# Performance work log

Measured on AMD Instinct MI355X. Metric: run time of the kernel, lower is better.

The kernel has to match this reference:

```python
import jax, jax.numpy as jnp
import numpy as np

N_NODES = 100000
N_EDGES = 1600000
N_GRAPHS = 512
IN_CH = 64
HID = 128
LAT = 64
MAX_NODES = 128
OUT_SIZE = MAX_NODES * (MAX_NODES - 1) // 2  # 8128


def _gcn_conv(x, W, b, src, dst, n):
    """PyG GCNConv: x' = D^-1/2 (A+I) D^-1/2 (x W) + b, degrees include self-loops."""
    h = x @ W  # [N, out]
    deg = jnp.zeros((n,), h.dtype).at[dst].add(1.0) + 1.0  # in-degree + self-loop
    dinv = jax.lax.rsqrt(deg)
    norm = dinv[src] * dinv[dst]  # [E]
    agg = jnp.zeros_like(h).at[dst].add(h[src] * norm[:, None])  # neighbor scatter-add
    agg = agg + h * (dinv * dinv)[:, None]  # self-loop term, norm = 1/deg
    return agg + b


def setup_inputs() -> dict:
    key = jax.random.key(0)
    ks = jax.random.split(key, 20)
    s = 0.02
    inp = {
        "x": jax.random.normal(ks[0], (N_NODES, IN_CH), jnp.float32),
        "edge_index": jax.random.randint(ks[1], (2, N_EDGES), 0, N_NODES),
        "batch": jnp.sort(jax.random.randint(ks[2], (N_NODES,), 0, N_GRAPHS)),
        "eps": jax.random.normal(ks[3], (N_GRAPHS, LAT), jnp.float32),
        # encoder params
        "W1": jax.random.normal(ks[4], (IN_CH, HID), jnp.float32) * s,
        "b1": jnp.zeros((HID,), jnp.float32),
        "W2": jax.random.normal(ks[5], (HID, HID), jnp.float32) * s,
        "b2": jnp.zeros((HID,), jnp.float32),
        "Wmu": jax.random.normal(ks[6], (HID, LAT), jnp.float32) * s,
        "bmu": jnp.zeros((LAT,), jnp.float32),
        "Wlv": jax.random.normal(ks[7], (HID, LAT), jnp.float32) * s,
        "blv": jnp.zeros((LAT,), jnp.float32),
        # decoder MLP params
        "D1": jax.random.normal(ks[8], (LAT, HID), jnp.float32) * s,
        "d1": jnp.zeros((HID,), jnp.float32),
        "D2": jax.random.normal(ks[9], (HID, HID), jnp.float32) * s,
        "d2": jnp.zeros((HID,), jnp.float32),
        "D3": jax.random.normal(ks[10], (HID, OUT_SIZE), jnp.float32) * s,
        "d3": jnp.zeros((OUT_SIZE,), jnp.float32),
    }
    return inp


def reference(x, edge_index, batch, eps, W1, b1, W2, b2, Wmu, bmu, Wlv, blv,
              D1, d1, D2, d2, D3, d3):
    src, dst = edge_index[0], edge_index[1]
    # --- encoder: two GCN layers + ReLU ---
    h = jax.nn.relu(_gcn_conv(x, W1, b1, src, dst, N_NODES))
    h = jax.nn.relu(_gcn_conv(h, W2, b2, src, dst, N_NODES))
    # --- global mean pool by graph id ---
    sums = jax.ops.segment_sum(h, batch, num_segments=N_GRAPHS)
    cnts = jax.ops.segment_sum(jnp.ones((N_NODES,), h.dtype), batch, num_segments=N_GRAPHS)
    h_graph = sums / jnp.maximum(cnts, 1.0)[:, None]  # [G, HID]
    mu = h_graph @ Wmu + bmu
    logvar = h_graph @ Wlv + blv
    # --- reparameterise ---
    z = mu + eps * jnp.exp(0.5 * logvar)  # [G, LAT]
    # --- MLP decoder -> symmetric adjacency ---
    p = jax.nn.relu(z @ D1 + d1)
    p = jax.nn.relu(p @ D2 + d2)
    probs = jax.nn.sigmoid(p @ D3 + d3)  # [G, OUT_SIZE]
    r, c = jnp.triu_indices(MAX_NODES, k=1)
    adj = jnp.zeros((N_GRAPHS, MAX_NODES, MAX_NODES), probs.dtype)
    adj = adj.at[:, r, c].set(probs)
    adj = adj + jnp.swapaxes(adj, 1, 2)
    return adj, mu, logvar
```

## Files before the change

### kernel.cpp

```cpp
#include <hip/hip_runtime.h>
#include <hip/hip_fp16.h>

#define NN 100000
#define NE 1600000
#define NG 512
#define OUTS 8128
#define NB2 196
#define CHUNK 8192
#define NPB 196

typedef short bf16x8 __attribute__((ext_vector_type(8)));
typedef _Float16 f16x8 __attribute__((ext_vector_type(8)));
typedef _Float16 f16x2 __attribute__((ext_vector_type(2)));
typedef float f32x4 __attribute__((ext_vector_type(4)));

__device__ __forceinline__ unsigned pack_bf16x2(float a, float b) {
    unsigned ua = __float_as_uint(a);
    unsigned ub = __float_as_uint(b);
    ua = (ua + 0x7fffu + ((ua >> 16) & 1u)) >> 16;
    ub = (ub + 0x7fffu + ((ub >> 16) & 1u)) >> 16;
    return ua | (ub << 16);
}
__device__ __forceinline__ unsigned short f2bf(float f) {
    unsigned u = __float_as_uint(f);
    u = (u + 0x7fffu + ((u >> 16) & 1u)) >> 16;
    return (unsigned short)u;
}
__device__ __forceinline__ unsigned cvt_pkrtz_u(float a, float b) {
    auto h = __builtin_amdgcn_cvt_pkrtz(a, b);
    union { decltype(h) h2; unsigned u; } c; c.h2 = h; return c.u;
}
__device__ __forceinline__ f16x2 u2h(unsigned u) { union { unsigned u; f16x2 h; } c; c.u = u; return c.h; }

__device__ __forceinline__ unsigned f2fp8(float f) {
    unsigned h = (unsigned)__half_as_ushort(__float2half(f * 0.00390625f));
    return (h + 0x3Fu + ((h >> 7) & 1u)) >> 7;
}

__global__ __launch_bounds__(512) void k_part(const int* __restrict__ src, const int* __restrict__ dst,
        int* __restrict__ tmp, int* __restrict__ scanhist) {
    __shared__ int hist[NB2], cur[NB2], scan[256];
    int p = blockIdx.x, t = threadIdx.x;
    int e0 = p * CHUNK;
    int e1 = min(e0 + CHUNK, NE);
    for (int i = t; i < NB2; i += 512) hist[i] = 0;
    __syncthreads();
    for (int e = e0 + t; e < e1; e += 512)
        atomicAdd(&hist[dst[e] >> 9], 1);
    __syncthreads();
    int h = 0;
    if (t < 256) { h = (t < NB2) ? hist[t] : 0; scan[t] = h; }
    __syncthreads();
    for (int off = 1; off < 256; off <<= 1) {
        int v = (t < 256 && t >= off) ? scan[t - off] : 0;
        __syncthreads();
        if (t < 256) scan[t] += v;
        __syncthreads();
    }
    if (t < NB2) {
        int excl = scan[t] - h;
        cur[t] = excl;
        scanhist[p * (NB2 + 1) + t] = excl;
    }
    if (t == 0) scanhist[p * (NB2 + 1) + NB2] = e1 - e0;
    __syncthreads();
    for (int e = e0 + t; e < e1; e += 512) {
        int d = dst[e];
        int b = d >> 9;
        int r = atomicAdd(&cur[b], 1);
        tmp[e0 + r] = (src[e] << 9) | (d & 511);
    }
}

__global__ __launch_bounds__(256) void k_btotseg(const int* __restrict__ scanhist,
        int* __restrict__ bucketbase, const int* __restrict__ batch, int* __restrict__ seg_end) {
    if (blockIdx.x == 0) {
        __shared__ int sc[256];
        int b = threadIdx.x;
        int tot = 0;
        if (b < NB2) {
            for (int p = 0; p < NPB; ++p)
                tot += scanhist[p * (NB2 + 1) + b + 1] - scanhist[p * (NB2 + 1) + b];
        }
        sc[b] = tot;
        __syncthreads();
        for (int off = 1; off < 256; off <<= 1) {
            int v = (b >= off) ? sc[b - off] : 0;
            __syncthreads();
            sc[b] += v;
            __syncthreads();
        }
        if (b < NB2) bucketbase[b] = sc[b] - tot;
    } else {
        int i = (blockIdx.x - 1) * 256 + threadIdx.x;
        if (i >= NN) return;
        int b = batch[i];
        int bn = (i == NN - 1) ? NG : batch[i + 1];
        for (int g = b; g < bn; ++g) seg_end[g] = i + 1;
        if (i == 0) {
            for (int g = 0; g < b; ++g) seg_end[g] = 0;
        }
    }
}

__global__ __launch_bounds__(1024) void k_fill2(const int* __restrict__ bucketbase,
        const int* __restrict__ scanhist, const int* __restrict__ tmp,
        int* __restrict__ colidx, int* __restrict__ cnti, int* __restrict__ rowptr,
        float* __restrict__ dinv) {
    __shared__ int lc[512], rb[512], sc[256];
    int b = blockIdx.x, t = threadIdx.x;
    int n0 = b << 9;
    if (t < 512) lc[t] = 0;
    __syncthreads();
    int w = t >> 6, lane = t & 63;
    for (int p = w; p < NPB; p += 16) {
        int s0 = scanhist[p * (NB2 + 1) + b];
        int s1 = scanhist[p * (NB2 + 1) + b + 1];
        int base = p * CHUNK;
        for (int i = s0 + lane; i < s1; i += 64)
            atomicAdd(&lc[tmp[base + i] & 511], 1);
    }
    __syncthreads();
    int v0 = 0, v1 = 0, s = 0;
    if (t < 256) { v0 = lc[2 * t]; v1 = lc[2 * t + 1]; s = v0 + v1; sc[t] = s; }
    __syncthreads();
    for (int off = 1; off < 256; off <<= 1) {
        int x = (t < 256 && t >= off) ? sc[t - off] : 0;
        __syncthreads();
        if (t < 256) sc[t] += x;
        __syncthreads();
    }
    if (t < 256) {
        int excl = sc[t] - s;
        int base0 = bucketbase[b];
        rb[2 * t] = base0 + excl;
        rb[2 * t + 1] = base0 + excl + v0;
        int node0 = n0 + 2 * t;
        if (node0 < NN) {
            cnti[node0] = v0;
            rowptr[node0] = base0 + excl;
            dinv[node0] = rsqrtf((float)v0 + 1.0f);
        }
        if (node0 + 1 < NN) {
            cnti[node0 + 1] = v1;
            rowptr[node0 + 1] = base0 + excl + v0;
            dinv[node0 + 1] = rsqrtf((float)v1 + 1.0f);
        }
    }
    __syncthreads();
    if (t < 512) lc[t] = 0;
    __syncthreads();
    for (int p = w; p < NPB; p += 16) {
        int s0 = scanhist[p * (NB2 + 1) + b];
        int s1 = scanhist[p * (NB2 + 1) + b + 1];
        int base = p * CHUNK;
        for (int i = s0 + lane; i < s1; i += 64) {
            int v = tmp[base + i];
            int dl = v & 511;
            int pos = atomicAdd(&lc[dl], 1);
            colidx[rb[dl] + pos] = v >> 9;
        }
    }
}

__global__ __launch_bounds__(256) void k_wtall(const float* __restrict__ W1,
        const float* __restrict__ W2,
        unsigned short* __restrict__ wt1, unsigned short* __restrict__ wt2) {
    int i = blockIdx.x * 256 + threadIdx.x;
    if (i < 8192) {
        int n = i >> 6, k = i & 63;
        wt1[i] = (unsigned short)__half_as_ushort(__float2half(W1[k * 128 + n]));
    } else if (i < 24576) {
        int e = i - 8192;
        int n = e >> 7, k = e & 127;
        wt2[e] = f2bf(W2[k * 128 + n]);
    }
}

__global__ __launch_bounds__(256) void k_wt3t(const float* __restrict__ D3,
        unsigned short* __restrict__ o) {
    __shared__ float tile[32][33];
    int n0 = blockIdx.x * 32, k0 = blockIdx.y * 32;
    for (int i = threadIdx.x; i < 1024; i += 256) {
        int kk = i >> 5, nn = i & 31;
        tile[kk][nn] = D3[(long)(k0 + kk) * OUTS + n0 + nn];
    }
    __syncthreads();
    for (int i = threadIdx.x; i < 1024; i += 256) {
        int nn = i >> 5, kk = i & 31;
        o[(long)(n0 + nn) * 128 + k0 + kk] =
            (unsigned short)__half_as_ushort(__float2half(tile[kk][nn]));
    }
}

__global__ __launch_bounds__(256) void k_scale_x(const float* __restrict__ x,
        const float* __restrict__ dinv, unsigned* __restrict__ u1) {
    int i = blockIdx.x * 256 + threadIdx.x;
    int row = i >> 5, c = i & 31;
    float2 v = *(const float2*)&x[(long)row * 64 + c * 2];
    float d = dinv[row];
    u1[i] = cvt_pkrtz_u(v.x * d, v.y * d);
}

__global__ __launch_bounds__(256) void k_gather1(const int* __restrict__ rowptr,
        const int* __restrict__ cnti, const int* __restrict__ colidx,
        const unsigned* __restrict__ u, const float* __restrict__ dinv,
        unsigned* __restrict__ s1) {
    int node = blockIdx.x * 32 + (threadIdx.x >> 3);
    int lane = threadIdx.x & 7;
    const uint4* uf = (const uint4*)u;
    uint4 self = uf[node * 8 + lane];
    f16x2 a0 = u2h(self.x), a1 = u2h(self.y), a2 = u2h(self.z), a3 = u2h(self.w);
    f16x2 z = {(_Float16)0.f, (_Float16)0.f};
    f16x2 b0 = z, b1 = z, b2 = z, b3 = z;
    int n = cnti[node];
    const int* ci = colidx + rowptr[node];
    int j = 0;
    for (; j + 4 <= n; j += 4) {
        uint4 va = uf[ci[j] * 8 + lane];
        uint4 vb = uf[ci[j + 1] * 8 + lane];
        uint4 vc = uf[ci[j + 2] * 8 + lane];
        uint4 vd = uf[ci[j + 3] * 8 + lane];
        a0 += u2h(va.x); a1 += u2h(va.y); a2 += u2h(va.z); a3 += u2h(va.w);
        b0 += u2h(vb.x); b1 += u2h(vb.y); b2 += u2h(vb.z); b3 += u2h(vb.w);
        a0 += u2h(vc.x); a1 += u2h(vc.y); a2 += u2h(vc.z); a3 += u2h(vc.w);
        b0 += u2h(vd.x); b1 += u2h(vd.y); b2 += u2h(vd.z); b3 += u2h(vd.w);
    }
    for (; j < n; ++j) {
        uint4 va = uf[ci[j] * 8 + lane];
        a0 += u2h(va.x); a1 += u2h(va.y); a2 += u2h(va.z); a3 += u2h(va.w);
    }
    a0 += b0; a1 += b1; a2 += b2; a3 += b3;
    float d = dinv[node];
    uint4 o;
    o.x = cvt_pkrtz_u((float)a0[0] * d, (float)a0[1] * d);
    o.y = cvt_pkrtz_u((float)a1[0] * d, (float)a1[1] * d);
    o.z = cvt_pkrtz_u((float)a2[0] * d, (float)a2[1] * d);
    o.w = cvt_pkrtz_u((float)a3[0] * d, (float)a3[1] * d);
    *(uint4*)&s1[node * 32 + lane * 4] = o;
}

#define DECO(W, LO, HI) { LO += u2h(((W) & 0x007f007fu) << 7); HI += u2h(((W) & 0x7f007f00u) >> 1); }
__global__ __launch_bounds__(256) void k_gather2(const int* __restrict__ rowptr,
        const int* __restrict__ cnti, const int* __restrict__ colidx,
        const unsigned* __restrict__ u, const float* __restrict__ dinv,
        unsigned* __restrict__ s2) {
    int node = blockIdx.x * 32 + (threadIdx.x >> 3);
    int lane = threadIdx.x & 7;
    const uint4* uf = (const uint4*)u;
    uint4 self = uf[node * 8 + lane];
    f16x2 z = {(_Float16)0.f, (_Float16)0.f};
    f16x2 la0 = z, ha0 = z, la1 = z, ha1 = z, la2 = z, ha2 = z, la3 = z, ha3 = z;
    f16x2 lb0 = z, hb0 = z, lb1 = z, hb1 = z, lb2 = z, hb2 = z, lb3 = z, hb3 = z;
    DECO(self.x, la0, ha0) DECO(self.y, la1, ha1) DECO(self.z, la2, ha2) DECO(self.w, la3, ha3)
    int n = cnti[node];
    const int* ci = colidx + rowptr[node];
    int j = 0;
    for (; j + 4 <= n; j += 4) {
        uint4 va = uf[ci[j] * 8 + lane];
        uint4 vb = uf[ci[j + 1] * 8 + lane];
        uint4 vc = uf[ci[j + 2] * 8 + lane];
        uint4 vd = uf[ci[j + 3] * 8 + lane];
        DECO(va.x, la0, ha0) DECO(va.y, la1, ha1) DECO(va.z, la2, ha2) DECO(va.w, la3, ha3)
        DECO(vb.x, lb0, hb0) DECO(vb.y, lb1, hb1) DECO(vb.z, lb2, hb2) DECO(vb.w, lb3, hb3)
        DECO(vc.x, la0, ha0) DECO(vc.y, la1, ha1) DECO(vc.z, la2, ha2) DECO(vc.w, la3, ha3)
        DECO(vd.x, lb0, hb0) DECO(vd.y, lb1, hb1) DECO(vd.z, lb2, hb2) DECO(vd.w, lb3, hb3)
    }
    for (; j < n; ++j) {
        uint4 va = uf[ci[j] * 8 + lane];
        DECO(va.x, la0, ha0) DECO(va.y, la1, ha1) DECO(va.z, la2, ha2) DECO(va.w, la3, ha3)
    }
    la0 += lb0; ha0 += hb0; la1 += lb1; ha1 += hb1;
    la2 += lb2; ha2 += hb2; la3 += lb3; ha3 += hb3;
    float d = dinv[node] * 16.0f;
    uint4 o1, o2;
    o1.x = pack_bf16x2((float)la0[0] * d, (float)ha0[0] * d);
    o1.y = pack_bf16x2((float)la0[1] * d, (float)ha0[1] * d);
    o1.z = pack_bf16x2((float)la1[0] * d, (float)ha1[0] * d);
    o1.w = pack_bf16x2((float)la1[1] * d, (float)ha1[1] * d);
    o2.x = pack_bf16x2((float)la2[0] * d, (float)ha2[0] * d);
    o2.y = pack_bf16x2((float)la2[1] * d, (float)ha2[1] * d);
    o2.z = pack_bf16x2((float)la3[0] * d, (float)ha3[0] * d);
    o2.w = pack_bf16x2((float)la3[1] * d, (float)ha3[1] * d);
    *(uint4*)&s2[node * 64 + lane * 8] = o1;
    *(uint4*)&s2[node * 64 + lane * 8 + 4] = o2;
}

template<int K, int EPI, int AF16>
__global__ __launch_bounds__(256) void k_gemm_mfma(const unsigned short* __restrict__ Ab,
        const unsigned short* __restrict__ wt, const float* __restrict__ dinv,
        const float* __restrict__ bias, void* __restrict__ outp) {
    constexpr int KS = K / 32;
    constexpr int SLOTS = K / 8;
    __shared__ __align__(16) unsigned short wlds[128 * K];
    char* lb = (char*)wlds;
    for (int c = threadIdx.x; c < 128 * SLOTS; c += 256) {
        int n = c / SLOTS, s = c - n * SLOTS;
        *(uint4*)(lb + n * (2 * K) + ((s ^ (n & 7)) << 4)) = *(const uint4*)(wt + c * 8);
    }
    __syncthreads();
    int lane = threadIdx.x & 63;
    int w = threadIdx.x >> 6;
    int r0 = blockIdx.x * 64 + w * 16;
    int arow = r0 + (lane & 15);
    if (arow >= NN) arow = NN - 1;
    bf16x8 af[KS];
    #pragma unroll
    for (int ks = 0; ks < KS; ++ks)
        af[ks] = *(const bf16x8*)&Ab[(long)arow * K + ks * 32 + (lane >> 4) * 8];
    f32x4 acc[8];
    #pragma unroll
    for (int t = 0; t < 8; ++t) acc[t] = (f32x4){0.f, 0.f, 0.f, 0.f};
    #pragma unroll
    for (int ks = 0; ks < KS; ++ks) {
        #pragma unroll
        for (int t = 0; t < 8; ++t) {
            int n = t * 16 + (lane & 15);
            int slot = ks * 4 + (lane >> 4);
            bf16x8 braw = *(const bf16x8*)(lb + n * (2 * K) + ((slot ^ (n & 7)) << 4));
            if constexpr (AF16) {
                union { bf16x8 r; f16x8 h; } ca, cb;
                ca.r = af[ks]; cb.r = braw;
                acc[t] = __builtin_amdgcn_mfma_f32_16x16x32_f16(ca.h, cb.h, acc[t], 0, 0, 0);
            } else {
                acc[t] = __builtin_amdgcn_mfma_f32_16x16x32_bf16(af[ks], braw, acc[t], 0, 0, 0);
            }
        }
    }
    float bv[8];
    #pragma unroll
    for (int t = 0; t < 8; ++t) bv[t] = bias[t * 16 + (lane & 15)];
    #pragma unroll
    for (int r = 0; r < 4; ++r) {
        long row = r0 + (lane >> 4) * 4 + r;
        if (row >= NN) continue;
        float d = dinv[row];
        #pragma unroll
        for (int t = 0; t < 8; ++t) {
            float val = fmaxf(acc[t][r] + bv[t], 0.f);
            int col = t * 16 + (lane & 15);
            if (EPI == 0)
                ((unsigned char*)outp)[row * 128 + col] = (unsigned char)f2fp8(val * (16.0f * d));
            else
                ((unsigned short*)outp)[row * 128 + col] = f2bf(val);
        }
    }
}

__global__ __launch_bounds__(256) void k_poolmean(const unsigned* __restrict__ h,
        const int* __restrict__ seg_end, float* __restrict__ hg) {
    __shared__ float part[3][128];
    int g = blockIdx.x;
    int w = threadIdx.x >> 6, t = threadIdx.x & 63;
    int s = (g == 0) ? 0 : seg_end[g - 1];
    int e = seg_end[g];
    float a0 = 0.f, a1 = 0.f;
    for (int i = s + w; i < e; i += 4) {
        unsigned u = h[(long)i * 64 + t];
        a0 += __uint_as_float(u << 16);
        a1 += __uint_as_float(u & 0xffff0000u);
    }
    if (w) { part[w - 1][t * 2] = a0; part[w - 1][t * 2 + 1] = a1; }
    __syncthreads();
    if (w == 0) {
        a0 += part[0][t * 2] + part[1][t * 2] + part[2][t * 2];
        a1 += part[0][t * 2 + 1] + part[1][t * 2 + 1] + part[2][t * 2 + 1];
        float inv = (e > s) ? 1.0f / (float)(e - s) : 0.f;
        float2 o = { a0 * inv, a1 * inv };
        *(float2*)&hg[g * 128 + t * 2] = o;
    }
}

__global__ __launch_bounds__(128) void k_decfused(const float* __restrict__ hg,
        const float* __restrict__ Wmu, const float* __restrict__ bmu,
        const float* __restrict__ Wlv, const float* __restrict__ blv,
        const float* __restrict__ eps,
        const float* __restrict__ D1, const float* __restrict__ d1,
        const float* __restrict__ D2, const float* __restrict__ d2,
        float* __restrict__ mu_o, float* __restrict__ lv_o,
        unsigned short* __restrict__ p2out) {
    __shared__ float row[128], mlv[128], zr[64], p1[128];
    int g = blockIdx.x, t = threadIdx.x;
    row[t] = hg[g * 128 + t];
    __syncthreads();
    if (t < 64) {
        float acc = bmu[t];
        for (int k = 0; k < 128; ++k) acc += row[k] * Wmu[k * 64 + t];
        mlv[t] = acc;
    } else {
        int t2 = t - 64;
        float acc = blv[t2];
        for (int k = 0; k < 128; ++k) acc += row[k] * Wlv[k * 64 + t2];
        mlv[64 + t2] = acc;
    }
    __syncthreads();
    if (t < 64) {
        float mu = mlv[t], lv = mlv[64 + t];
        mu_o[g * 64 + t] = mu;
        lv_o[g * 64 + t] = lv;
        zr[t] = mu + eps[g * 64 + t] * expf(0.5f * lv);
    }
    __syncthreads();
    float acc = d1[t];
    for (int k = 0; k < 64; ++k) acc += zr[k] * D1[k * 128 + t];
    p1[t] = fmaxf(acc, 0.f);
    __syncthreads();
    acc = d2[t];
    for (int k = 0; k < 128; ++k) acc += p1[k] * D2[k * 128 + t];
    p2out[g * 128 + t] = (unsigned short)__half_as_ushort(__float2half(fmaxf(acc, 0.f)));
}

__global__ __launch_bounds__(256) void k_dec3m(const unsigned short* __restrict__ Ab,
        const unsigned short* __restrict__ Wt, const float* __restrict__ b,
        float* __restrict__ out) {
    int lane = threadIdx.x & 63;
    int w = threadIdx.x >> 6;
    int r0 = blockIdx.x * 64 + w * 16;
    int c0 = blockIdx.y * 64;
    int arow = r0 + (lane & 15);
    f16x8 af[4];
    #pragma unroll
    for (int ks = 0; ks < 4; ++ks) {
        union { bf16x8 r; f16x8 h; } ca;
        ca.r = *(const bf16x8*)&Ab[arow * 128 + ks * 32 + (lane >> 4) * 8];
        af[ks] = ca.h;
    }
    f32x4 acc[4];
    #pragma unroll
    for (int nt = 0; nt < 4; ++nt) acc[nt] = (f32x4){0.f, 0.f, 0.f, 0.f};
    #pragma unroll
    for (int nt = 0; nt < 4; ++nt) {
        long n = c0 + nt * 16 + (lane & 15);
        #pragma unroll
        for (int ks = 0; ks < 4; ++ks) {
            union { bf16x8 r; f16x8 h; } cb;
            cb.r = *(const bf16x8*)&Wt[n * 128 + ks * 32 + (lane >> 4) * 8];
            acc[nt] = __builtin_amdgcn_mfma_f32_16x16x32_f16(af[ks], cb.h, acc[nt], 0, 0, 0);
        }
    }
    #pragma unroll
    for (int nt = 0; nt < 4; ++nt) {
        int col = c0 + nt * 16 + (lane & 15);
        float bias = b[col];
        #pragma unroll
        for (int r = 0; r < 4; ++r) {
            int row = r0 + (lane >> 4) * 4 + r;
            float v = acc[nt][r] + bias;
            out[(long)row * OUTS + col] = 1.f / (1.f + expf(-v));
        }
    }
}

__global__ __launch_bounds__(256) void k_adj(const float* __restrict__ probs, float* __restrict__ adj) {
    int t = blockIdx.x * 256 + threadIdx.x;
    int g = t >> 12;
    int rem = t & 4095;
    int r = rem >> 5;
    int c0 = (rem & 31) * 4;
    const float* pg = &probs[g * OUTS];
    float4 o;
    float* op = (float*)&o;
    #pragma unroll
    for (int j = 0; j < 4; ++j) {
        int c = c0 + j;
        if (c == r) { op[j] = 0.f; continue; }
        int a = c < r ? c : r;
        int b = c < r ? r : c;
        int k = a * (255 - a) / 2 + (b - a - 1);
        op[j] = pg[k];
    }
    *(float4*)&adj[(long)t * 4] = o;
}

extern "C" void kernel_launch(void* const* d_in, const int* in_sizes, int n_in,
                              void* d_out, int out_size, void* d_ws, size_t ws_size,
                              hipStream_t stream) {
    const float* x   = (const float*)d_in[0];
    const int*   ei  = (const int*)d_in[1];
    const int* batch = (const int*)d_in[2];
    const float* eps = (const float*)d_in[3];
    const float* W1  = (const float*)d_in[4];
    const float* b1  = (const float*)d_in[5];
    const float* W2  = (const float*)d_in[6];
    const float* b2  = (const float*)d_in[7];
    const float* Wmu = (const float*)d_in[8];
    const float* bmu = (const float*)d_in[9];
    const float* Wlv = (const float*)d_in[10];
    const float* blv = (const float*)d_in[11];
    const float* D1  = (const float*)d_in[12];
    const float* d1  = (const float*)d_in[13];
    const float* D2  = (const float*)d_in[14];
    const float* d2  = (const float*)d_in[15];
    const float* D3  = (const float*)d_in[16];
    const float* d3  = (const float*)d_in[17];

    const int* esrc = ei;
    const int* edst = ei + NE;

    float* out  = (float*)d_out;
    float* mu_o = out + 8388608;
    float* lv_o = mu_o + 32768;

    int*   colidx   = (int*)out;
    int*   cnti     = colidx + 1600000;
    int*   rowptr   = cnti + 100000;
    int*   seg_end  = rowptr + 100000;
    float* dinv     = (float*)(seg_end + 512);
    int*   scanhist = (int*)(dinv + 100000);
    int*   bucketbase = scanhist + 38612;
    unsigned short* wt3t = (unsigned short*)(bucketbase + 256);

    float* ws = (float*)d_ws;
    unsigned* u1u = (unsigned*)ws;
    unsigned* s1u = u1u + 3200000;
    unsigned char* u2b = (unsigned char*)(ws + 6400000);
    unsigned* s2u = (unsigned*)(ws + 9600000);
    unsigned* h2b = (unsigned*)(ws + 16000000);
    unsigned short* wt1 = (unsigned short*)(ws + 22400000);
    unsigned short* wt2 = wt1 + 8192;
    int* tmp = (int*)(ws + 22420000);
    float* hg = ws;
    unsigned short* p2b = (unsigned short*)(hg + 65536);
    float* probs = hg + 131072;

    k_part<<<NPB, 512, 0, stream>>>(esrc, edst, tmp, scanhist);
    k_btotseg<<<392, 256, 0, stream>>>(scanhist, bucketbase, batch, seg_end);
    k_fill2<<<NB2, 1024, 0, stream>>>(bucketbase, scanhist, tmp, colidx, cnti, rowptr, dinv);

    k_wtall<<<96, 256, 0, stream>>>(W1, W2, wt1, wt2);
    dim3 gt(254, 4);
    k_wt3t<<<gt, 256, 0, stream>>>(D3, wt3t);

    k_scale_x<<<12500, 256, 0, stream>>>(x, dinv, u1u);
    k_gather1<<<3125, 256, 0, stream>>>(rowptr, cnti, colidx, u1u, dinv, s1u);
    k_gemm_mfma<64, 0, 1><<<1563, 256, 0, stream>>>((const unsigned short*)s1u, wt1, dinv, b1, u2b);

    k_gather2<<<3125, 256, 0, stream>>>(rowptr, cnti, colidx, (const unsigned*)u2b, dinv, s2u);
    k_gemm_mfma<128, 1, 0><<<1563, 256, 0, stream>>>((const unsigned short*)s2u, wt2, dinv, b2, h2b);

    k_poolmean<<<NG, 256, 0, stream>>>(h2b, seg_end, hg);
    k_decfused<<<NG, 128, 0, stream>>>(hg, Wmu, bmu, Wlv, blv, eps, D1, d1, D2, d2,
                                       mu_o, lv_o, p2b);

    dim3 g3(8, 127);
    k_dec3m<<<g3, 256, 0, stream>>>(p2b, wt3t, d3, probs);
    k_adj<<<8192, 256, 0, stream>>>(probs, out);
}
```

Measured before the change: 220.6 us.

## Store scaled layer-1 input as signed fp8 and fuse setup and pooling kernels

Layer-1 neighbor features are now packed as signed 8-bit floats (fp16 bit-truncation with a 1/256 prescale), and that packing is computed inside k_fill2, which removes the separate k_scale_x kernel. The gather reads them at half the previous byte width, with 4 lanes per node instead of 8. The weight-transpose kernels are merged into one launch, and the pooling kernel is fused with the decoder head so the hg round-trip goes away. In exchange, layer-1 inputs lose precision and k_fill2 takes on extra work, which lengthens its critical path.

After: 205.7 us. 1.07x faster.

```diff
diff --git a/kernel.cpp b/kernel.cpp
--- a/kernel.cpp
+++ b/kernel.cpp
@@ -36,6 +36,17 @@
     unsigned h = (unsigned)__half_as_ushort(__float2half(f * 0.00390625f));
     return (h + 0x3Fu + ((h >> 7) & 1u)) >> 7;
 }
+__device__ __forceinline__ unsigned f2fp8s(float f) {
+    unsigned h = (unsigned)__half_as_ushort(__float2half(f * 0.00390625f));
+    unsigned s = (h >> 8) & 0x80u;
+    unsigned mag = h & 0x7fffu;
+    return s | ((mag + 0x3Fu + ((mag >> 7) & 1u)) >> 7);
+}
+
+#define DECO(W, LO, HI) { LO += u2h(((W) & 0x007f007fu) << 7); HI += u2h(((W) & 0x7f007f00u) >> 1); }
+#define DECOS(W, LO, HI) { \
+    LO += u2h((((W) & 0x007f007fu) << 7) | (((W) & 0x00800080u) << 8)); \
+    HI += u2h((((W) & 0x7f007f00u) >> 1) | ((W) & 0x80008000u)); }
 
 __global__ __launch_bounds__(512) void k_part(const int* __restrict__ src, const int* __restrict__ dst,
         int* __restrict__ tmp, int* __restrict__ scanhist) {
@@ -106,8 +117,9 @@
 __global__ __launch_bounds__(1024) void k_fill2(const int* __restrict__ bucketbase,
         const int* __restrict__ scanhist, const int* __restrict__ tmp,
         int* __restrict__ colidx, int* __restrict__ cnti, int* __restrict__ rowptr,
-        float* __restrict__ dinv) {
+        float* __restrict__ dinv, const float* __restrict__ x, unsigned* __restrict__ u1b) {
     __shared__ int lc[512], rb[512], sc[256];
+    __shared__ float ldv[512];
     int b = blockIdx.x, t = threadIdx.x;
     int n0 = b << 9;
     if (t < 512) lc[t] = 0;
@@ -125,9 +137,9 @@
     if (t < 256) { v0 = lc[2 * t]; v1 = lc[2 * t + 1]; s = v0 + v1; sc[t] = s; }
     __syncthreads();
     for (int off = 1; off < 256; off <<= 1) {
-        int x = (t < 256 && t >= off) ? sc[t - off] : 0;
+        int xv = (t < 256 && t >= off) ? sc[t - off] : 0;
         __syncthreads();
-        if (t < 256) sc[t] += x;
+        if (t < 256) sc[t] += xv;
         __syncthreads();
     }
     if (t < 256) {
@@ -135,16 +147,20 @@
         int base0 = bucketbase[b];
         rb[2 * t] = base0 + excl;
         rb[2 * t + 1] = base0 + excl + v0;
+        float dv0 = rsqrtf((float)v0 + 1.0f);
+        float dv1 = rsqrtf((float)v1 + 1.0f);
+        ldv[2 * t] = dv0;
+        ldv[2 * t + 1] = dv1;
         int node0 = n0 + 2 * t;
         if (node0 < NN) {
             cnti[node0] = v0;
             rowptr[node0] = base0 + excl;
-            dinv[node0] = rsqrtf((float)v0 + 1.0f);
+            dinv[node0] = dv0;
         }
         if (node0 + 1 < NN) {
             cnti[node0 + 1] = v1;
             rowptr[node0 + 1] = base0 + excl + v0;
-            dinv[node0 + 1] = rsqrtf((float)v1 + 1.0f);
+            dinv[node0 + 1] = dv1;
         }
     }
     __syncthreads();
@@ -161,86 +177,96 @@
             colidx[rb[dl] + pos] = v >> 9;
         }
     }
+    for (int i = t; i < 512 * 16; i += 1024) {
+        int local = i >> 4, c = i & 15;
+        int node = n0 + local;
+        if (node >= NN) continue;
+        float4 xv = *(const float4*)&x[(long)node * 64 + c * 4];
+        float d = ldv[local];
+        unsigned o = f2fp8s(xv.x * d) | (f2fp8s(xv.y * d) << 8)
+                   | (f2fp8s(xv.z * d) << 16) | (f2fp8s(xv.w * d) << 24);
+        u1b[node * 16 + c] = o;
+    }
 }
 
 __global__ __launch_bounds__(256) void k_wtall(const float* __restrict__ W1,
-        const float* __restrict__ W2,
-        unsigned short* __restrict__ wt1, unsigned short* __restrict__ wt2) {
-    int i = blockIdx.x * 256 + threadIdx.x;
-    if (i < 8192) {
-        int n = i >> 6, k = i & 63;
-        wt1[i] = (unsigned short)__half_as_ushort(__float2half(W1[k * 128 + n]));
-    } else if (i < 24576) {
-        int e = i - 8192;
-        int n = e >> 7, k = e & 127;
-        wt2[e] = f2bf(W2[k * 128 + n]);
-    }
-}
-
-__global__ __launch_bounds__(256) void k_wt3t(const float* __restrict__ D3,
-        unsigned short* __restrict__ o) {
+        const float* __restrict__ W2, const float* __restrict__ D3,
+        unsigned short* __restrict__ wt1, unsigned short* __restrict__ wt2,
+        unsigned short* __restrict__ wt3t) {
     __shared__ float tile[32][33];
-    int n0 = blockIdx.x * 32, k0 = blockIdx.y * 32;
-    for (int i = threadIdx.x; i < 1024; i += 256) {
-        int kk = i >> 5, nn = i & 31;
-        tile[kk][nn] = D3[(long)(k0 + kk) * OUTS + n0 + nn];
-    }
-    __syncthreads();
-    for (int i = threadIdx.x; i < 1024; i += 256) {
-        int nn = i >> 5, kk = i & 31;
-        o[(long)(n0 + nn) * 128 + k0 + kk] =
-            (unsigned short)__half_as_ushort(__float2half(tile[kk][nn]));
-    }
-}
-
-__global__ __launch_bounds__(256) void k_scale_x(const float* __restrict__ x,
-        const float* __restrict__ dinv, unsigned* __restrict__ u1) {
-    int i = blockIdx.x * 256 + threadIdx.x;
-    int row = i >> 5, c = i & 31;
-    float2 v = *(const float2*)&x[(long)row * 64 + c * 2];
-    float d = dinv[row];
-    u1[i] = cvt_pkrtz_u(v.x * d, v.y * d);
+    int blk = blockIdx.x;
+    if (blk < 96) {
+        int i = blk * 256 + threadIdx.x;
+        if (i < 8192) {
+            int n = i >> 6, k = i & 63;
+            wt1[i] = (unsigned short)__half_as_ushort(__float2half(W1[k * 128 + n]));
+        } else {
+            int e = i - 8192;
+            int n = e >> 7, k = e & 127;
+            wt2[e] = f2bf(W2[k * 128 + n]);
+        }
+    } else {
+        int bb = blk - 96;
+        int n0 = (bb % 254) * 32, k0 = (bb / 254) * 32;
+        for (int i = threadIdx.x; i < 1024; i += 256) {
+            int kk = i >> 5, nn = i & 31;
+            tile[kk][nn] = D3[(long)(k0 + kk) * OUTS + n0 + nn];
+        }
+        __syncthreads();
+        for (int i = threadIdx.x; i < 1024; i += 256) {
+            int nn = i >> 5, kk = i & 31;
+            wt3t[(long)(n0 + nn) * 128 + k0 + kk] =
+                (unsigned short)__half_as_ushort(__float2half(tile[kk][nn]));
+        }
+    }
 }
 
 __global__ __launch_bounds__(256) void k_gather1(const int* __restrict__ rowptr,
         const int* __restrict__ cnti, const int* __restrict__ colidx,
         const unsigned* __restrict__ u, const float* __restrict__ dinv,
         unsigned* __restrict__ s1) {
-    int node = blockIdx.x * 32 + (threadIdx.x >> 3);
-    int lane = threadIdx.x & 7;
+    int node = blockIdx.x * 64 + (threadIdx.x >> 2);
+    if (node >= NN) return;
+    int lane = threadIdx.x & 3;
     const uint4* uf = (const uint4*)u;
-    uint4 self = uf[node * 8 + lane];
-    f16x2 a0 = u2h(self.x), a1 = u2h(self.y), a2 = u2h(self.z), a3 = u2h(self.w);
+    uint4 self = uf[node * 4 + lane];
     f16x2 z = {(_Float16)0.f, (_Float16)0.f};
-    f16x2 b0 = z, b1 = z, b2 = z, b3 = z;
+    f16x2 la0 = z, ha0 = z, la1 = z, ha1 = z, la2 = z, ha2 = z, la3 = z, ha3 = z;
+    f16x2 lb0 = z, hb0 = z, lb1 = z, hb1 = z, lb2 = z, hb2 = z, lb3 = z, hb3 = z;
+    DECOS(self.x, la0, ha0) DECOS(self.y, la1, ha1) DECOS(self.z, la2, ha2) DECOS(self.w, la3, ha3)
     int n = cnti[node];
     const int* ci = colidx + rowptr[node];
     int j = 0;
     for (; j + 4 <= n; j += 4) {
-        uint4 va = uf[ci[j] * 8 + lane];
-        uint4 vb = uf[ci[j + 1] * 8 + lane];
-        uint4 vc = uf[ci[j + 2] * 8 + lane];
-        uint4 vd = uf[ci[j + 3] * 8 + lane];
-        a0 += u2h(va.x); a1 += u2h(va.y); a2 += u2h(va.z); a3 += u2h(va.w);
-        b0 += u2h(vb.x); b1 += u2h(vb.y); b2 += u2h(vb.z); b3 += u2h(vb.w);
-        a0 += u2h(vc.x); a1 += u2h(vc.y); a2 += u2h(vc.z); a3 += u2h(vc.w);
-        b0 += u2h(vd.x); b1 += u2h(vd.y); b2 += u2h(vd.z); b3 += u2h(vd.w);
+        uint4 va = uf[ci[j] * 4 + lane];
+        uint4 vb = uf[ci[j + 1] * 4 + lane];
+        uint4 vc = uf[ci[j + 2] * 4 + lane];
+        uint4 vd = uf[ci[j + 3] * 4 + lane];
+        DECOS(va.x, la0, ha0) DECOS(va.y, la1, ha1) DECOS(va.z, la2, ha2) DECOS(va.w, la3, ha3)
+        DECOS(vb.x, lb0, hb0) DECOS(vb.y, lb1, hb1) DECOS(vb.z, lb2, hb2) DECOS(vb.w, lb3, hb3)
+        DECOS(vc.x, la0, ha0) DECOS(vc.y, la1, ha1) DECOS(vc.z, la2, ha2) DECOS(vc.w, la3, ha3)
+        DECOS(vd.x, lb0, hb0) DECOS(vd.y, lb1, hb1) DECOS(vd.z, lb2, hb2) DECOS(vd.w, lb3, hb3)
     }
     for (; j < n; ++j) {
-        uint4 va = uf[ci[j] * 8 + lane];
-        a0 += u2h(va.x); a1 += u2h(va.y); a2 += u2h(va.z); a3 += u2h(va.w);
-    }
-    a0 += b0; a1 += b1; a2 += b2; a3 += b3;
-    float d = dinv[node];
-    uint4 o;
-    o.x = cvt_pkrtz_u((float)a0[0] * d, (float)a0[1] * d);
-    o.y = cvt_pkrtz_u((float)a1[0] * d, (float)a1[1] * d);
-    o.z = cvt_pkrtz_u((float)a2[0] * d, (float)a2[1] * d);
-    o.w = cvt_pkrtz_u((float)a3[0] * d, (float)a3[1] * d);
-    *(uint4*)&s1[node * 32 + lane * 4] = o;
-}
-
-#define DECO(W, LO, HI) { LO += u2h(((W) & 0x007f007fu) << 7); HI += u2h(((W) & 0x7f007f00u) >> 1); }
+        uint4 va = uf[ci[j] * 4 + lane];
+        DECOS(va.x, la0, ha0) DECOS(va.y, la1, ha1) DECOS(va.z, la2, ha2) DECOS(va.w, la3, ha3)
+    }
+    la0 += lb0; ha0 += hb0; la1 += lb1; ha1 += hb1;
+    la2 += lb2; ha2 += hb2; la3 += lb3; ha3 += hb3;
+    float d = dinv[node] * 256.0f;
+    uint4 o1, o2;
+    o1.x = cvt_pkrtz_u((float)la0[0] * d, (float)ha0[0] * d);
+    o1.y = cvt_pkrtz_u((float)la0[1] * d, (float)ha0[1] * d);
+    o1.z = cvt_pkrtz_u((float)la1[0] * d, (float)ha1[0] * d);
+    o1.w = cvt_pkrtz_u((float)la1[1] * d, (float)ha1[1] * d);
+    o2.x = cvt_pkrtz_u((float)la2[0] * d, (float)ha2[0] * d);
+    o2.y = cvt_pkrtz_u((float)la2[1] * d, (float)ha2[1] * d);
+    o2.z = cvt_pkrtz_u((float)la3[0] * d, (float)ha3[0] * d);
+    o2.w = cvt_pkrtz_u((float)la3[1] * d, (float)ha3[1] * d);
+    *(uint4*)&s1[node * 32 + lane * 8] = o1;
+    *(uint4*)&s1[node * 32 + lane * 8 + 4] = o2;
+}
+
 __global__ __launch_bounds__(256) void k_gather2(const int* __restrict__ rowptr,
         const int* __restrict__ cnti, const int* __restrict__ colidx,
         const unsigned* __restrict__ u, const float* __restrict__ dinv,
@@ -347,31 +373,8 @@
     }
 }
 
-__global__ __launch_bounds__(256) void k_poolmean(const unsigned* __restrict__ h,
-        const int* __restrict__ seg_end, float* __restrict__ hg) {
-    __shared__ float part[3][128];
-    int g = blockIdx.x;
-    int w = threadIdx.x >> 6, t = threadIdx.x & 63;
-    int s = (g == 0) ? 0 : seg_end[g - 1];
-    int e = seg_end[g];
-    float a0 = 0.f, a1 = 0.f;
-    for (int i = s + w; i < e; i += 4) {
-        unsigned u = h[(long)i * 64 + t];
-        a0 += __uint_as_float(u << 16);
-        a1 += __uint_as_float(u & 0xffff0000u);
-    }
-    if (w) { part[w - 1][t * 2] = a0; part[w - 1][t * 2 + 1] = a1; }
-    __syncthreads();
-    if (w == 0) {
-        a0 += part[0][t * 2] + part[1][t * 2] + part[2][t * 2];
-        a1 += part[0][t * 2 + 1] + part[1][t * 2 + 1] + part[2][t * 2 + 1];
-        float inv = (e > s) ? 1.0f / (float)(e - s) : 0.f;
-        float2 o = { a0 * inv, a1 * inv };
-        *(float2*)&hg[g * 128 + t * 2] = o;
-    }
-}
-
-__global__ __launch_bounds__(128) void k_decfused(const float* __restrict__ hg,
+__global__ __launch_bounds__(256) void k_pooldec(const unsigned* __restrict__ h,
+        const int* __restrict__ seg_end,
         const float* __restrict__ Wmu, const float* __restrict__ bmu,
         const float* __restrict__ Wlv, const float* __restrict__ blv,
         const float* __restrict__ eps,
@@ -379,15 +382,34 @@
         const float* __restrict__ D2, const float* __restrict__ d2,
         float* __restrict__ mu_o, float* __restrict__ lv_o,
         unsigned short* __restrict__ p2out) {
+    __shared__ float part[3][128];
     __shared__ float row[128], mlv[128], zr[64], p1[128];
-    int g = blockIdx.x, t = threadIdx.x;
-    row[t] = hg[g * 128 + t];
-    __syncthreads();
+    int g = blockIdx.x;
+    int w = threadIdx.x >> 6, t64 = threadIdx.x & 63;
+    int s = (g == 0) ? 0 : seg_end[g - 1];
+    int e = seg_end[g];
+    float a0 = 0.f, a1 = 0.f;
+    for (int i = s + w; i < e; i += 4) {
+        unsigned u = h[(long)i * 64 + t64];
+        a0 += __uint_as_float(u << 16);
+        a1 += __uint_as_float(u & 0xffff0000u);
+    }
+    if (w) { part[w - 1][t64 * 2] = a0; part[w - 1][t64 * 2 + 1] = a1; }
+    __syncthreads();
+    if (w == 0) {
+        a0 += part[0][t64 * 2] + part[1][t64 * 2] + part[2][t64 * 2];
+        a1 += part[0][t64 * 2 + 1] + part[1][t64 * 2 + 1] + part[2][t64 * 2 + 1];
+        float inv = (e > s) ? 1.0f / (float)(e - s) : 0.f;
+        row[t64 * 2] = a0 * inv;
+        row[t64 * 2 + 1] = a1 * inv;
+    }
+    __syncthreads();
+    int t = threadIdx.x;
     if (t < 64) {
         float acc = bmu[t];
         for (int k = 0; k < 128; ++k) acc += row[k] * Wmu[k * 64 + t];
         mlv[t] = acc;
-    } else {
+    } else if (t < 128) {
         int t2 = t - 64;
         float acc = blv[t2];
         for (int k = 0; k < 128; ++k) acc += row[k] * Wlv[k * 64 + t2];
@@ -401,13 +423,17 @@
         zr[t] = mu + eps[g * 64 + t] * expf(0.5f * lv);
     }
     __syncthreads();
-    float acc = d1[t];
-    for (int k = 0; k < 64; ++k) acc += zr[k] * D1[k * 128 + t];
-    p1[t] = fmaxf(acc, 0.f);
-    __syncthreads();
-    acc = d2[t];
-    for (int k = 0; k < 128; ++k) acc += p1[k] * D2[k * 128 + t];
-    p2out[g * 128 + t] = (unsigned short)__half_as_ushort(__float2half(fmaxf(acc, 0.f)));
+    if (t < 128) {
+        float acc = d1[t];
+        for (int k = 0; k < 64; ++k) acc += zr[k] * D1[k * 128 + t];
+        p1[t] = fmaxf(acc, 0.f);
+    }
+    __syncthreads();
+    if (t < 128) {
+        float acc = d2[t];
+        for (int k = 0; k < 128; ++k) acc += p1[k] * D2[k * 128 + t];
+        p2out[g * 128 + t] = (unsigned short)__half_as_ushort(__float2half(fmaxf(acc, 0.f)));
+    }
 }
 
 __global__ __launch_bounds__(256) void k_dec3m(const unsigned short* __restrict__ Ab,
@@ -511,36 +537,32 @@
     unsigned short* wt3t = (unsigned short*)(bucketbase + 256);
 
     float* ws = (float*)d_ws;
-    unsigned* u1u = (unsigned*)ws;
-    unsigned* s1u = u1u + 3200000;
+    unsigned* u1b = (unsigned*)ws;
+    unsigned* s1u = (unsigned*)(ws + 3200000);
     unsigned char* u2b = (unsigned char*)(ws + 6400000);
     unsigned* s2u = (unsigned*)(ws + 9600000);
     unsigned* h2b = (unsigned*)(ws + 16000000);
     unsigned short* wt1 = (unsigned short*)(ws + 22400000);
     unsigned short* wt2 = wt1 + 8192;
     int* tmp = (int*)(ws + 22420000);
-    float* hg = ws;
-    unsigned short* p2b = (unsigned short*)(hg + 65536);
-    float* probs = hg + 131072;
+    unsigned short* p2b = (unsigned short*)ws;
+    float* probs = ws + 65536;
 
     k_part<<<NPB, 512, 0, stream>>>(esrc, edst, tmp, scanhist);
     k_btotseg<<<392, 256, 0, stream>>>(scanhist, bucketbase, batch, seg_end);
-    k_fill2<<<NB2, 1024, 0, stream>>>(bucketbase, scanhist, tmp, colidx, cnti, rowptr, dinv);
-
-    k_wtall<<<96, 256, 0, stream>>>(W1, W2, wt1, wt2);
-    dim3 gt(254, 4);
-    k_wt3t<<<gt, 256, 0, stream>>>(D3, wt3t);
-
-    k_scale_x<<<12500, 256, 0, stream>>>(x, dinv, u1u);
-    k_gather1<<<3125, 256, 0, stream>>>(rowptr, cnti, colidx, u1u, dinv, s1u);
+    k_fill2<<<NB2, 1024, 0, stream>>>(bucketbase, scanhist, tmp, colidx, cnti, rowptr,
+                                      dinv, x, u1b);
+
+    k_wtall<<<1112, 256, 0, stream>>>(W1, W2, D3, wt1, wt2, wt3t);
+
+    k_gather1<<<1563, 256, 0, stream>>>(rowptr, cnti, colidx, u1b, dinv, s1u);
     k_gemm_mfma<64, 0, 1><<<1563, 256, 0, stream>>>((const unsigned short*)s1u, wt1, dinv, b1, u2b);
 
     k_gather2<<<3125, 256, 0, stream>>>(rowptr, cnti, colidx, (const unsigned*)u2b, dinv, s2u);
     k_gemm_mfma<128, 1, 0><<<1563, 256, 0, stream>>>((const unsigned short*)s2u, wt2, dinv, b2, h2b);
 
-    k_poolmean<<<NG, 256, 0, stream>>>(h2b, seg_end, hg);
-    k_decfused<<<NG, 128, 0, stream>>>(hg, Wmu, bmu, Wlv, blv, eps, D1, d1, D2, d2,
-                                       mu_o, lv_o, p2b);
+    k_pooldec<<<NG, 256, 0, stream>>>(h2b, seg_end, Wmu, bmu, Wlv, blv, eps,
+                                      D1, d1, D2, d2, mu_o, lv_o, p2b);
 
     dim3 g3(8, 127);
     k_dec3m<<<g3, 256, 0, stream>>>(p2b, wt3t, d3, probs);
```
